# Optimization experiments

Measured on AMD Instinct MI355X. Metric: run time of the kernel, lower is better.

## Reference

```python
import jax, jax.numpy as jnp
import numpy as np

N_STATE, N_OBS, BATCH, T_LEN = 256, 128, 64, 1024
RICCATI_ITERS = 300


def _steady_state_gain(A, H, Q, R, iters=RICCATI_ITERS):
    """Riccati iteration for the steady-state Kalman gain (numpy, fp64)."""
    n = A.shape[0]
    I = np.eye(n)
    P = np.eye(n)
    for _ in range(iters):
        Pp = A @ P @ A.T + Q
        S = H @ Pp @ H.T + R
        K = np.linalg.solve(S, (Pp @ H.T).T).T
        P = (I - K @ H) @ Pp
    return K


def setup_inputs() -> dict:
    rng = np.random.default_rng(0)
    # Stable dynamics: scaled orthogonal matrix (spectral radius 0.95).
    M = rng.standard_normal((N_STATE, N_STATE))
    Qm, _ = np.linalg.qr(M)
    A = 0.95 * Qm
    H = rng.standard_normal((N_OBS, N_STATE)) / np.sqrt(N_STATE)
    Qc = 0.1 * np.eye(N_STATE)
    Rc = 0.1 * np.eye(N_OBS)
    K = _steady_state_gain(A, H, Qc, Rc)

    key = jax.random.key(0)
    y = jax.random.normal(key, (BATCH, T_LEN, N_OBS), dtype=jnp.float32)
    return {
        "y": y,
        "A": jnp.asarray(A, dtype=jnp.float32),
        "H": jnp.asarray(H, dtype=jnp.float32),
        "K": jnp.asarray(K, dtype=jnp.float32),
    }


def reference(y, A, H, K):
    """Steady-state Kalman filter: x_t = (I - K H) A x_{t-1} + K y_t.

    y: [B, T, n_obs] -> out: [B, T, n_state]
    """
    n = A.shape[0]
    I = jnp.eye(n, dtype=A.dtype)
    A_eff = (I - K @ H) @ A  # [n, n]

    x0 = y[:, 0] @ K.T  # [B, n]

    def step(x, yt):
        x = x @ A_eff.T + yt @ K.T  # [B, n]
        return x, x

    ys = jnp.swapaxes(y[:, 1:], 0, 1)  # [T-1, B, n_obs]
    _, xs = jax.lax.scan(step, x0, ys)  # xs: [T-1, B, n]
    out = jnp.concatenate([x0[:, None, :], jnp.swapaxes(xs, 0, 1)], axis=1)
    return out  # [B, T, n_state]
```

## Files before the change

### kernel.cpp

```cpp
#include <hip/hip_runtime.h>

#define NS 256
#define MO 128
#define BB 64
#define TT 1024
#define CCH 64
#define SS 16

typedef short s16x8 __attribute__((ext_vector_type(8)));
typedef float f32x4 __attribute__((ext_vector_type(4)));
typedef unsigned int uint;
typedef unsigned short ushort;

__device__ __forceinline__ ushort f2bf(float x) {
    uint u = __float_as_uint(x);
    uint r = (u + 0x7fffu + ((u >> 16) & 1u)) >> 16;
    return (ushort)r;
}
__device__ __forceinline__ float bf2f(ushort h) { return __uint_as_float(((uint)h) << 16); }

__device__ __forceinline__ f32x4 mfma16(s16x8 a, s16x8 b, f32x4 c) {
    return __builtin_amdgcn_mfma_f32_16x16x32_bf16(a, b, c, 0, 0, 0);
}


__global__ void kh_kernel(const float* __restrict__ K, const float* __restrict__ H,
                          float* __restrict__ KH) {
    int i = blockIdx.x, j = threadIdx.x;
    __shared__ float kl[MO];
    if (j < MO) kl[j] = K[i * MO + j];
    __syncthreads();
    float acc = 0.f;
#pragma unroll 8
    for (int k = 0; k < MO; ++k) acc += kl[k] * H[k * NS + j];
    KH[i * NS + j] = acc;
}

__global__ void aeff_kernel(const float* __restrict__ A, const float* __restrict__ KH,
                            float* __restrict__ AE) {
    int i = blockIdx.x, j = threadIdx.x;
    __shared__ float khr[NS];
    khr[j] = KH[i * NS + j];
    __syncthreads();
    float acc = A[i * NS + j];
#pragma unroll 8
    for (int k = 0; k < NS; ++k) acc -= khr[k] * A[k * NS + j];
    AE[i * NS + j] = acc;
}

__global__ void matsq_kernel(const float* __restrict__ src, float* __restrict__ dst) {
    int i = blockIdx.x, j = threadIdx.x;
    __shared__ float row[NS];
    row[j] = src[i * NS + j];
    __syncthreads();
    float acc = 0.f;
#pragma unroll 8
    for (int k = 0; k < NS; ++k) acc += row[k] * src[k * NS + j];
    dst[i * NS + j] = acc;
}

__global__ void conv_kernel(const float* __restrict__ AE, const float* __restrict__ M,
                            const float* __restrict__ M2,
                            ushort* __restrict__ aeh, ushort* __restrict__ ael,
                            ushort* __restrict__ mh, ushort* __restrict__ ml,
                            ushort* __restrict__ m2h, ushort* __restrict__ m2l) {
    int i = (blockIdx.x & 255) * 256 + threadIdx.x;
    int mat = blockIdx.x >> 8;
    const float* src = (mat == 0) ? AE : ((mat == 1) ? M : M2);
    ushort* dh = (mat == 0) ? aeh : ((mat == 1) ? mh : m2h);
    ushort* dl = (mat == 0) ? ael : ((mat == 1) ? ml : m2l);
    float v = src[i];
    ushort hi = f2bf(v);
    dh[i] = hi;
    dl[i] = f2bf(v - bf2f(hi));
}


__launch_bounds__(512, 2)
__global__ void ugemm_kernel(const float* __restrict__ y, const float* __restrict__ K,
                             float* __restrict__ U) {
    const int tid = threadIdx.x, blk = blockIdx.x;
    const int w = tid >> 6, l = tid & 63, lr = l & 15, lg = l >> 4;

    s16x8 KBh[2][4], KBl[2][4];
#pragma unroll
    for (int t2 = 0; t2 < 2; ++t2) {
        int row = 16 * (2 * w + t2) + lr;
#pragma unroll
        for (int q = 0; q < 4; ++q) {
            int off = row * MO + 32 * q + 8 * lg;
            float4 a = *(const float4*)(K + off);
            float4 b = *(const float4*)(K + off + 4);
            s16x8 vh, vl;
            float f;
            ushort h;
            f = a.x; h = f2bf(f); vh[0] = (short)h; vl[0] = (short)f2bf(f - bf2f(h));
            f = a.y; h = f2bf(f); vh[1] = (short)h; vl[1] = (short)f2bf(f - bf2f(h));
            f = a.z; h = f2bf(f); vh[2] = (short)h; vl[2] = (short)f2bf(f - bf2f(h));
            f = a.w; h = f2bf(f); vh[3] = (short)h; vl[3] = (short)f2bf(f - bf2f(h));
            f = b.x; h = f2bf(f); vh[4] = (short)h; vl[4] = (short)f2bf(f - bf2f(h));
            f = b.y; h = f2bf(f); vh[5] = (short)h; vl[5] = (short)f2bf(f - bf2f(h));
            f = b.z; h = f2bf(f); vh[6] = (short)h; vl[6] = (short)f2bf(f - bf2f(h));
            f = b.w; h = f2bf(f); vh[7] = (short)h; vl[7] = (short)f2bf(f - bf2f(h));
            KBh[t2][q] = vh; KBl[t2][q] = vl;
        }
    }

#pragma unroll 1
    for (int it = 0; it < 16; ++it) {
        int rt = blk * 16 + it;
        s16x8 Ah[4], Al[4];
#pragma unroll
        for (int q = 0; q < 4; ++q) {
            int off = (rt * 16 + lr) * MO + 32 * q + 8 * lg;
            float4 a = *(const float4*)(y + off);
            float4 b = *(const float4*)(y + off + 4);
            s16x8 vh, vl;
            float f;
            ushort h;
            f = a.x; h = f2bf(f); vh[0] = (short)h; vl[0] = (short)f2bf(f - bf2f(h));
            f = a.y; h = f2bf(f); vh[1] = (short)h; vl[1] = (short)f2bf(f - bf2f(h));
            f = a.z; h = f2bf(f); vh[2] = (short)h; vl[2] = (short)f2bf(f - bf2f(h));
            f = a.w; h = f2bf(f); vh[3] = (short)h; vl[3] = (short)f2bf(f - bf2f(h));
            f = b.x; h = f2bf(f); vh[4] = (short)h; vl[4] = (short)f2bf(f - bf2f(h));
            f = b.y; h = f2bf(f); vh[5] = (short)h; vl[5] = (short)f2bf(f - bf2f(h));
            f = b.z; h = f2bf(f); vh[6] = (short)h; vl[6] = (short)f2bf(f - bf2f(h));
            f = b.w; h = f2bf(f); vh[7] = (short)h; vl[7] = (short)f2bf(f - bf2f(h));
            Ah[q] = vh; Al[q] = vl;
        }
        f32x4 acc0 = {0.f, 0.f, 0.f, 0.f};
        f32x4 acc1 = {0.f, 0.f, 0.f, 0.f};
#pragma unroll
        for (int q = 0; q < 4; ++q) {
            acc0 = mfma16(Ah[q], KBh[0][q], acc0);
            acc0 = mfma16(Al[q], KBh[0][q], acc0);
            acc0 = mfma16(Ah[q], KBl[0][q], acc0);
            acc1 = mfma16(Ah[q], KBh[1][q], acc1);
            acc1 = mfma16(Al[q], KBh[1][q], acc1);
            acc1 = mfma16(Ah[q], KBl[1][q], acc1);
        }
#pragma unroll
        for (int i = 0; i < 4; ++i) {
            int orow = rt * 16 + 4 * lg + i;
            U[orow * NS + 32 * w + lr] = acc0[i];
            U[orow * NS + 32 * w + 16 + lr] = acc1[i];
        }
    }
}


template <int MODE>
__launch_bounds__(512, 2)
__global__ void scan16_kernel(const ushort* __restrict__ mh, const ushort* __restrict__ ml,
                              const float* u, const float* __restrict__ cin,
                              float* wout, float* __restrict__ eout) {
    constexpr int S = (MODE == 0 || MODE == 4) ? SS : 8;
    const int tid = threadIdx.x;
    const int blk = blockIdx.x;
    const int w = tid >> 6;
    const int l = tid & 63;
    const int lr = l & 15;
    const int lg = l >> 4;

    __shared__ ushort xh_s[16 * NS];
    __shared__ ushort xl_s[16 * NS];

    auto ubase = [&](int m) -> long {
        if constexpr (MODE == 0 || MODE == 4) {
            int cc = blk >> 2, b = (blk & 3) * 16 + m;
            return ((long)b * TT + cc * SS) * NS;
        } else if constexpr (MODE == 1 || MODE == 3) {
            int rid = blk * 16 + m;
            int b = rid >> 3, g = rid & 7;
            return ((long)b * 64 + g * 8) * NS;
        } else {
            int b = blk * 16 + m;
            return (long)b * 8 * NS;
        }
    };

    s16x8 Bh[2][8], Bl[2][8];
#pragma unroll
    for (int t2 = 0; t2 < 2; ++t2) {
        int row = 16 * (2 * w + t2) + lr;
#pragma unroll
        for (int q = 0; q < 8; ++q) {
            int off = row * NS + 32 * q + 8 * lg;
            Bh[t2][q] = *(const s16x8*)(mh + off);
            Bl[t2][q] = *(const s16x8*)(ml + off);
        }
    }

#pragma unroll
    for (int jj = 0; jj < 8; ++jj) {
        int idx = jj * 512 + tid;
        int m = idx >> 8, col = idx & 255;
        float xv = 0.f;
        if constexpr (MODE == 3) {
            int rid = blk * 16 + m;
            int b = rid >> 3, g = rid & 7;
            xv = cin[(b * 8 + g) * NS + col];
            if (g == 0) wout[(long)b * 64 * NS + col] = 0.f;
        } else if constexpr (MODE == 4) {
            int cc = blk >> 2, b = (blk & 3) * 16 + m;
            xv = cin[(b * 64 + cc) * NS + col];
        } else if constexpr (MODE == 2) {
            int b = blk * 16 + m;
            wout[(long)b * 8 * NS + col] = 0.f;
        }
        ushort hi = f2bf(xv);
        ushort lo = f2bf(xv - bf2f(hi));
        int sidx = (m * NS + col) ^ ((m & 7) << 3);
        xh_s[sidx] = hi;
        xl_s[sidx] = lo;
    }

    const int col0 = 32 * w + lr;
    const int col1 = col0 + 16;

    float up0[4], up1[4];
#pragma unroll
    for (int i = 0; i < 4; ++i) {
        int m = 4 * lg + i;
        long ub = ubase(m);
        up0[i] = u[ub + col0];
        up1[i] = u[ub + col1];
    }
    __syncthreads();

    for (int s = 0; s < S; ++s) {
        f32x4 acc0, acc1;
        acc0[0] = up0[0]; acc0[1] = up0[1]; acc0[2] = up0[2]; acc0[3] = up0[3];
        acc1[0] = up1[0]; acc1[1] = up1[1]; acc1[2] = up1[2]; acc1[3] = up1[3];

#pragma unroll
        for (int q = 0; q < 8; ++q) {
            int ridx = (lr * NS + 32 * q + 8 * lg) ^ ((lr & 7) << 3);
            s16x8 xh = *(const s16x8*)&xh_s[ridx];
            s16x8 xl = *(const s16x8*)&xl_s[ridx];
            acc0 = mfma16(xh, Bh[0][q], acc0);
            acc0 = mfma16(xl, Bh[0][q], acc0);
            acc0 = mfma16(xh, Bl[0][q], acc0);
            acc1 = mfma16(xh, Bh[1][q], acc1);
            acc1 = mfma16(xl, Bh[1][q], acc1);
            acc1 = mfma16(xh, Bl[1][q], acc1);
        }

        if (s + 1 < S) {
#pragma unroll
            for (int i = 0; i < 4; ++i) {
                int m = 4 * lg + i;
                long ub = ubase(m) + (long)(s + 1) * NS;
                up0[i] = u[ub + col0];
                up1[i] = u[ub + col1];
            }
        }

        if constexpr (MODE == 2) {
            if (s < 7) {
#pragma unroll
                for (int i = 0; i < 4; ++i) {
                    int m = 4 * lg + i;
                    int b = blk * 16 + m;
                    long wb = ((long)b * 8 + s + 1) * NS;
                    wout[wb + col0] = acc0[i];
                    wout[wb + col1] = acc1[i];
                }
            }
        } else if constexpr (MODE == 3) {
#pragma unroll
            for (int i = 0; i < 4; ++i) {
                int m = 4 * lg + i;
                int rid = blk * 16 + m;
                int b = rid >> 3, g = rid & 7;
                int kk = 8 * g + s + 1;
                if (kk < 64) {
                    long wb = ((long)b * 64 + kk) * NS;
                    wout[wb + col0] = acc0[i];
                    wout[wb + col1] = acc1[i];
                }
            }
        } else if constexpr (MODE == 4) {
#pragma unroll
            for (int i = 0; i < 4; ++i) {
                int m = 4 * lg + i;
                long wb = ubase(m) + (long)s * NS;
                wout[wb + col0] = acc0[i];
                wout[wb + col1] = acc1[i];
            }
        }
        if constexpr (MODE == 0 || MODE == 1) {
            if (s == S - 1) {
#pragma unroll
                for (int i = 0; i < 4; ++i) {
                    int m = 4 * lg + i;
                    long eb;
                    if constexpr (MODE == 0) {
                        int cc = blk >> 2, b = (blk & 3) * 16 + m;
                        eb = ((long)b * 64 + cc) * NS;
                    } else {
                        eb = (long)(blk * 16 + m) * NS;
                    }
                    eout[eb + col0] = acc0[i];
                    eout[eb + col1] = acc1[i];
                }
            }
        }

        __syncthreads();

#pragma unroll
        for (int i = 0; i < 4; ++i) {
            int m = 4 * lg + i;
            {
                ushort hi = f2bf(acc0[i]);
                ushort lo = f2bf(acc0[i] - bf2f(hi));
                int wi = (m * NS + col0) ^ ((m & 7) << 3);
                xh_s[wi] = hi;
                xl_s[wi] = lo;
            }
            {
                ushort hi = f2bf(acc1[i]);
                ushort lo = f2bf(acc1[i] - bf2f(hi));
                int wi = (m * NS + col1) ^ ((m & 7) << 3);
                xh_s[wi] = hi;
                xl_s[wi] = lo;
            }
        }
        __syncthreads();
    }
}


extern "C" void kernel_launch(void* const* d_in, const int* in_sizes, int n_in,
                              void* d_out, int out_size, void* d_ws, size_t ws_size,
                              hipStream_t stream) {
    const float* y = (const float*)d_in[0];
    const float* A = (const float*)d_in[1];
    const float* H = (const float*)d_in[2];
    const float* K = (const float*)d_in[3];
    float* out = (float*)d_out;

    float* ws = (float*)d_ws;
    const long MAT = (long)NS * NS;
    float* KH = ws + 0 * MAT;
    float* AE = ws + 1 * MAT;
    float* W0 = ws + 2 * MAT;
    float* W1 = ws + 3 * MAT;
    float* W2 = ws + 4 * MAT;
    float* W3 = ws + 5 * MAT;
    float* W4 = ws + 6 * MAT;
    float* W5 = ws + 7 * MAT;
    float* W6 = ws + 8 * MAT;
    ushort* aeh = (ushort*)(ws + 9 * MAT);
    ushort* ael = aeh + MAT;
    ushort* mh = ael + MAT;
    ushort* ml = mh + MAT;
    ushort* m2h = ml + MAT;
    ushort* m2l = m2h + MAT;
    float* e_buf = ws + 12 * MAT;
    float* e2 = ws + 28 * MAT;
    float* c2 = ws + 30 * MAT;
    float* cbuf = ws + 32 * MAT;

    float* U = out;

    kh_kernel<<<NS, NS, 0, stream>>>(K, H, KH);
    aeff_kernel<<<NS, NS, 0, stream>>>(A, KH, AE);
    matsq_kernel<<<NS, NS, 0, stream>>>(AE, W0);
    matsq_kernel<<<NS, NS, 0, stream>>>(W0, W1);
    matsq_kernel<<<NS, NS, 0, stream>>>(W1, W2);
    matsq_kernel<<<NS, NS, 0, stream>>>(W2, W3);
    matsq_kernel<<<NS, NS, 0, stream>>>(W3, W4);
    matsq_kernel<<<NS, NS, 0, stream>>>(W4, W5);
    matsq_kernel<<<NS, NS, 0, stream>>>(W5, W6);
    conv_kernel<<<768, 256, 0, stream>>>(AE, W3, W6, aeh, ael, mh, ml, m2h, m2l);

    ugemm_kernel<<<256, 512, 0, stream>>>(y, K, U);

    scan16_kernel<0><<<256, 512, 0, stream>>>(aeh, ael, U, nullptr, nullptr, e_buf);
    scan16_kernel<1><<<32, 512, 0, stream>>>(mh, ml, e_buf, nullptr, nullptr, e2);
    scan16_kernel<2><<<4, 512, 0, stream>>>(m2h, m2l, e2, nullptr, c2, nullptr);
    scan16_kernel<3><<<32, 512, 0, stream>>>(mh, ml, e_buf, c2, cbuf, nullptr);
    scan16_kernel<4><<<256, 512, 0, stream>>>(aeh, ael, U, cbuf, out, nullptr);
}
```

Measured before the change: 249.5 us.

## Fuse input-projection GEMM into chunked scan kernels, recompute y·Kᵀ on the fly

Removes the separate ugemm kernel that wrote U = y·Kᵀ to the output buffer. The first and last scan passes now stream y into double-buffered shared memory, split it into bf16 hi/lo, and compute the K projection with MFMA before applying the state transition. K is pre-split to bf16 hi/lo once in the conversion kernel. The final pass stages its results in shared memory so it can write them to global memory with coalesced float4 stores. This avoids writing and re-reading the large U tensor and saves a launch, at the cost of doing the projection twice (in both y-consuming passes) and using more shared memory, which may lower occupancy.

```diff
diff --git a/kernel.cpp b/kernel.cpp
--- a/kernel.cpp
+++ b/kernel.cpp
@@ -1,4 +1,5 @@
 #include <hip/hip_runtime.h>
+#include <hip/hip_bf16.h>
 
 #define NS 256
 #define MO 128
@@ -18,6 +19,32 @@
     return (ushort)r;
 }
 __device__ __forceinline__ float bf2f(ushort h) { return __uint_as_float(((uint)h) << 16); }
+
+__device__ __forceinline__ uint pkbf2(float a, float b) {
+    __hip_bfloat162 h = __float22bfloat162_rn(make_float2(a, b));
+    union { __hip_bfloat162 b2; uint u; } cv;
+    cv.b2 = h;
+    return cv.u;
+}
+
+__device__ __forceinline__ void conv8(float4 f0, float4 f1, s16x8& vh, s16x8& vl) {
+    uint h0 = pkbf2(f0.x, f0.y), h1 = pkbf2(f0.z, f0.w);
+    uint h2 = pkbf2(f1.x, f1.y), h3 = pkbf2(f1.z, f1.w);
+    float r0 = f0.x - __uint_as_float(h0 << 16);
+    float r1 = f0.y - __uint_as_float(h0 & 0xffff0000u);
+    float r2 = f0.z - __uint_as_float(h1 << 16);
+    float r3 = f0.w - __uint_as_float(h1 & 0xffff0000u);
+    float r4 = f1.x - __uint_as_float(h2 << 16);
+    float r5 = f1.y - __uint_as_float(h2 & 0xffff0000u);
+    float r6 = f1.z - __uint_as_float(h3 << 16);
+    float r7 = f1.w - __uint_as_float(h3 & 0xffff0000u);
+    uint l0 = pkbf2(r0, r1), l1 = pkbf2(r2, r3);
+    uint l2 = pkbf2(r4, r5), l3 = pkbf2(r6, r7);
+    union { uint u[4]; s16x8 v; } ch, cl;
+    ch.u[0] = h0; ch.u[1] = h1; ch.u[2] = h2; ch.u[3] = h3;
+    cl.u[0] = l0; cl.u[1] = l1; cl.u[2] = l2; cl.u[3] = l3;
+    vh = ch.v; vl = cl.v;
+}
 
 __device__ __forceinline__ f32x4 mfma16(s16x8 a, s16x8 b, f32x4 c) {
     return __builtin_amdgcn_mfma_f32_16x16x32_bf16(a, b, c, 0, 0, 0);
@@ -60,12 +87,22 @@
 }
 
 __global__ void conv_kernel(const float* __restrict__ AE, const float* __restrict__ M,
-                            const float* __restrict__ M2,
+                            const float* __restrict__ M2, const float* __restrict__ K,
                             ushort* __restrict__ aeh, ushort* __restrict__ ael,
                             ushort* __restrict__ mh, ushort* __restrict__ ml,
-                            ushort* __restrict__ m2h, ushort* __restrict__ m2l) {
-    int i = (blockIdx.x & 255) * 256 + threadIdx.x;
-    int mat = blockIdx.x >> 8;
+                            ushort* __restrict__ m2h, ushort* __restrict__ m2l,
+                            ushort* __restrict__ kbh, ushort* __restrict__ kbl) {
+    int blk = blockIdx.x;
+    if (blk >= 768) {
+        int i = (blk - 768) * 256 + threadIdx.x;
+        float v = K[i];
+        ushort hi = f2bf(v);
+        kbh[i] = hi;
+        kbl[i] = f2bf(v - bf2f(hi));
+        return;
+    }
+    int i = (blk & 255) * 256 + threadIdx.x;
+    int mat = blk >> 8;
     const float* src = (mat == 0) ? AE : ((mat == 1) ? M : M2);
     ushort* dh = (mat == 0) ? aeh : ((mat == 1) ? mh : m2h);
     ushort* dl = (mat == 0) ? ael : ((mat == 1) ? ml : m2l);
@@ -76,85 +113,15 @@
 }
 
 
-__launch_bounds__(512, 2)
-__global__ void ugemm_kernel(const float* __restrict__ y, const float* __restrict__ K,
-                             float* __restrict__ U) {
-    const int tid = threadIdx.x, blk = blockIdx.x;
-    const int w = tid >> 6, l = tid & 63, lr = l & 15, lg = l >> 4;
-
-    s16x8 KBh[2][4], KBl[2][4];
-#pragma unroll
-    for (int t2 = 0; t2 < 2; ++t2) {
-        int row = 16 * (2 * w + t2) + lr;
-#pragma unroll
-        for (int q = 0; q < 4; ++q) {
-            int off = row * MO + 32 * q + 8 * lg;
-            float4 a = *(const float4*)(K + off);
-            float4 b = *(const float4*)(K + off + 4);
-            s16x8 vh, vl;
-            float f;
-            ushort h;
-            f = a.x; h = f2bf(f); vh[0] = (short)h; vl[0] = (short)f2bf(f - bf2f(h));
-            f = a.y; h = f2bf(f); vh[1] = (short)h; vl[1] = (short)f2bf(f - bf2f(h));
-            f = a.z; h = f2bf(f); vh[2] = (short)h; vl[2] = (short)f2bf(f - bf2f(h));
-            f = a.w; h = f2bf(f); vh[3] = (short)h; vl[3] = (short)f2bf(f - bf2f(h));
-            f = b.x; h = f2bf(f); vh[4] = (short)h; vl[4] = (short)f2bf(f - bf2f(h));
-            f = b.y; h = f2bf(f); vh[5] = (short)h; vl[5] = (short)f2bf(f - bf2f(h));
-            f = b.z; h = f2bf(f); vh[6] = (short)h; vl[6] = (short)f2bf(f - bf2f(h));
-            f = b.w; h = f2bf(f); vh[7] = (short)h; vl[7] = (short)f2bf(f - bf2f(h));
-            KBh[t2][q] = vh; KBl[t2][q] = vl;
-        }
-    }
-
-#pragma unroll 1
-    for (int it = 0; it < 16; ++it) {
-        int rt = blk * 16 + it;
-        s16x8 Ah[4], Al[4];
-#pragma unroll
-        for (int q = 0; q < 4; ++q) {
-            int off = (rt * 16 + lr) * MO + 32 * q + 8 * lg;
-            float4 a = *(const float4*)(y + off);
-            float4 b = *(const float4*)(y + off + 4);
-            s16x8 vh, vl;
-            float f;
-            ushort h;
-            f = a.x; h = f2bf(f); vh[0] = (short)h; vl[0] = (short)f2bf(f - bf2f(h));
-            f = a.y; h = f2bf(f); vh[1] = (short)h; vl[1] = (short)f2bf(f - bf2f(h));
-            f = a.z; h = f2bf(f); vh[2] = (short)h; vl[2] = (short)f2bf(f - bf2f(h));
-            f = a.w; h = f2bf(f); vh[3] = (short)h; vl[3] = (short)f2bf(f - bf2f(h));
-            f = b.x; h = f2bf(f); vh[4] = (short)h; vl[4] = (short)f2bf(f - bf2f(h));
-            f = b.y; h = f2bf(f); vh[5] = (short)h; vl[5] = (short)f2bf(f - bf2f(h));
-            f = b.z; h = f2bf(f); vh[6] = (short)h; vl[6] = (short)f2bf(f - bf2f(h));
-            f = b.w; h = f2bf(f); vh[7] = (short)h; vl[7] = (short)f2bf(f - bf2f(h));
-            Ah[q] = vh; Al[q] = vl;
-        }
-        f32x4 acc0 = {0.f, 0.f, 0.f, 0.f};
-        f32x4 acc1 = {0.f, 0.f, 0.f, 0.f};
-#pragma unroll
-        for (int q = 0; q < 4; ++q) {
-            acc0 = mfma16(Ah[q], KBh[0][q], acc0);
-            acc0 = mfma16(Al[q], KBh[0][q], acc0);
-            acc0 = mfma16(Ah[q], KBl[0][q], acc0);
-            acc1 = mfma16(Ah[q], KBh[1][q], acc1);
-            acc1 = mfma16(Al[q], KBh[1][q], acc1);
-            acc1 = mfma16(Ah[q], KBl[1][q], acc1);
-        }
-#pragma unroll
-        for (int i = 0; i < 4; ++i) {
-            int orow = rt * 16 + 4 * lg + i;
-            U[orow * NS + 32 * w + lr] = acc0[i];
-            U[orow * NS + 32 * w + 16 + lr] = acc1[i];
-        }
-    }
-}
-
-
 template <int MODE>
 __launch_bounds__(512, 2)
 __global__ void scan16_kernel(const ushort* __restrict__ mh, const ushort* __restrict__ ml,
+                              const ushort* __restrict__ kbh, const ushort* __restrict__ kbl,
+                              const float* __restrict__ y_g,
                               const float* u, const float* __restrict__ cin,
                               float* wout, float* __restrict__ eout) {
-    constexpr int S = (MODE == 0 || MODE == 4) ? SS : 8;
+    constexpr bool YF = (MODE == 0 || MODE == 4);
+    constexpr int S = YF ? SS : 8;
     const int tid = threadIdx.x;
     const int blk = blockIdx.x;
     const int w = tid >> 6;
@@ -164,12 +131,15 @@
 
     __shared__ ushort xh_s[16 * NS];
     __shared__ ushort xl_s[16 * NS];
+    __shared__ float ybuf[2][16 * MO];
+    __shared__ float xe_s[16 * NS];
+
+    const int b0 = (blk & 3) * 16;
+    const int cc = blk >> 2;
+    const int t0 = cc * SS;
 
     auto ubase = [&](int m) -> long {
-        if constexpr (MODE == 0 || MODE == 4) {
-            int cc = blk >> 2, b = (blk & 3) * 16 + m;
-            return ((long)b * TT + cc * SS) * NS;
-        } else if constexpr (MODE == 1 || MODE == 3) {
+        if constexpr (MODE == 1 || MODE == 3) {
             int rid = blk * 16 + m;
             int b = rid >> 3, g = rid & 7;
             return ((long)b * 64 + g * 8) * NS;
@@ -188,6 +158,20 @@
             int off = row * NS + 32 * q + 8 * lg;
             Bh[t2][q] = *(const s16x8*)(mh + off);
             Bl[t2][q] = *(const s16x8*)(ml + off);
+        }
+    }
+
+    s16x8 KBh[2][4], KBl[2][4];
+    if constexpr (YF) {
+#pragma unroll
+        for (int t2 = 0; t2 < 2; ++t2) {
+            int row = 16 * (2 * w + t2) + lr;
+#pragma unroll
+            for (int q = 0; q < 4; ++q) {
+                int off = row * MO + 32 * q + 8 * lg;
+                KBh[t2][q] = *(const s16x8*)(kbh + off);
+                KBl[t2][q] = *(const s16x8*)(kbl + off);
+            }
         }
     }
 
@@ -202,8 +186,7 @@
             xv = cin[(b * 8 + g) * NS + col];
             if (g == 0) wout[(long)b * 64 * NS + col] = 0.f;
         } else if constexpr (MODE == 4) {
-            int cc = blk >> 2, b = (blk & 3) * 16 + m;
-            xv = cin[(b * 64 + cc) * NS + col];
+            xv = cin[((long)(b0 + m) * 64 + cc) * NS + col];
         } else if constexpr (MODE == 2) {
             int b = blk * 16 + m;
             wout[(long)b * 8 * NS + col] = 0.f;
@@ -218,20 +201,55 @@
     const int col0 = 32 * w + lr;
     const int col1 = col0 + 16;
 
+    const int yr = tid >> 5;
+    const int yc = (tid & 31) << 2;
+    const float* ysrc = nullptr;
+    int ywbyte = 0;
+    float4 vnext = make_float4(0.f, 0.f, 0.f, 0.f);
+    if constexpr (YF) {
+        ysrc = y_g + ((size_t)(b0 + yr) * TT + t0) * MO + yc;
+        ywbyte = (yr * 512 + yc * 4) ^ ((yr & 7) << 4);
+        float4 v0 = *(const float4*)(ysrc);
+        *(float4*)((char*)(&ybuf[0][0]) + ywbyte) = v0;
+        vnext = *(const float4*)(ysrc + MO);
+    }
+
     float up0[4], up1[4];
-#pragma unroll
-    for (int i = 0; i < 4; ++i) {
-        int m = 4 * lg + i;
-        long ub = ubase(m);
-        up0[i] = u[ub + col0];
-        up1[i] = u[ub + col1];
+    if constexpr (!YF) {
+#pragma unroll
+        for (int i = 0; i < 4; ++i) {
+            int m = 4 * lg + i;
+            long ub = ubase(m);
+            up0[i] = u[ub + col0];
+            up1[i] = u[ub + col1];
+        }
     }
     __syncthreads();
 
     for (int s = 0; s < S; ++s) {
         f32x4 acc0, acc1;
-        acc0[0] = up0[0]; acc0[1] = up0[1]; acc0[2] = up0[2]; acc0[3] = up0[3];
-        acc1[0] = up1[0]; acc1[1] = up1[1]; acc1[2] = up1[2]; acc1[3] = up1[3];
+        if constexpr (YF) {
+            acc0 = f32x4{0.f, 0.f, 0.f, 0.f};
+            acc1 = f32x4{0.f, 0.f, 0.f, 0.f};
+            const char* yb = (const char*)(&ybuf[s & 1][0]);
+#pragma unroll
+            for (int q = 0; q < 4; ++q) {
+                int lb = lr * 512 + q * 128 + lg * 32;
+                float4 f0 = *(const float4*)(yb + (lb ^ ((lr & 7) << 4)));
+                float4 f1 = *(const float4*)(yb + ((lb + 16) ^ ((lr & 7) << 4)));
+                s16x8 yh, yl;
+                conv8(f0, f1, yh, yl);
+                acc0 = mfma16(yh, KBh[0][q], acc0);
+                acc0 = mfma16(yl, KBh[0][q], acc0);
+                acc0 = mfma16(yh, KBl[0][q], acc0);
+                acc1 = mfma16(yh, KBh[1][q], acc1);
+                acc1 = mfma16(yl, KBh[1][q], acc1);
+                acc1 = mfma16(yh, KBl[1][q], acc1);
+            }
+        } else {
+            acc0[0] = up0[0]; acc0[1] = up0[1]; acc0[2] = up0[2]; acc0[3] = up0[3];
+            acc1[0] = up1[0]; acc1[1] = up1[1]; acc1[2] = up1[2]; acc1[3] = up1[3];
+        }
 
 #pragma unroll
         for (int q = 0; q < 8; ++q) {
@@ -246,13 +264,15 @@
             acc1 = mfma16(xh, Bl[1][q], acc1);
         }
 
-        if (s + 1 < S) {
-#pragma unroll
-            for (int i = 0; i < 4; ++i) {
-                int m = 4 * lg + i;
-                long ub = ubase(m) + (long)(s + 1) * NS;
-                up0[i] = u[ub + col0];
-                up1[i] = u[ub + col1];
+        if constexpr (!YF) {
+            if (s + 1 < S) {
+#pragma unroll
+                for (int i = 0; i < 4; ++i) {
+                    int m = 4 * lg + i;
+                    long ub = ubase(m) + (long)(s + 1) * NS;
+                    up0[i] = u[ub + col0];
+                    up1[i] = u[ub + col1];
+                }
             }
         }
 
@@ -280,14 +300,6 @@
                     wout[wb + col1] = acc1[i];
                 }
             }
-        } else if constexpr (MODE == 4) {
-#pragma unroll
-            for (int i = 0; i < 4; ++i) {
-                int m = 4 * lg + i;
-                long wb = ubase(m) + (long)s * NS;
-                wout[wb + col0] = acc0[i];
-                wout[wb + col1] = acc1[i];
-            }
         }
         if constexpr (MODE == 0 || MODE == 1) {
             if (s == S - 1) {
@@ -296,8 +308,7 @@
                     int m = 4 * lg + i;
                     long eb;
                     if constexpr (MODE == 0) {
-                        int cc = blk >> 2, b = (blk & 3) * 16 + m;
-                        eb = ((long)b * 64 + cc) * NS;
+                        eb = ((long)(b0 + m) * 64 + cc) * NS;
                     } else {
                         eb = (long)(blk * 16 + m) * NS;
                     }
@@ -326,8 +337,30 @@
                 xh_s[wi] = hi;
                 xl_s[wi] = lo;
             }
+            if constexpr (MODE == 4) {
+                xe_s[(m * NS + col0) ^ ((m & 7) << 2)] = acc0[i];
+                xe_s[(m * NS + col1) ^ ((m & 7) << 2)] = acc1[i];
+            }
+        }
+        if constexpr (YF) {
+            if (s + 1 < S) {
+                *(float4*)((char*)(&ybuf[(s + 1) & 1][0]) + ywbyte) = vnext;
+                if (s + 2 < S) vnext = *(const float4*)(ysrc + (size_t)(s + 2) * MO);
+            }
         }
         __syncthreads();
+
+        if constexpr (MODE == 4) {
+#pragma unroll
+            for (int j = 0; j < 2; ++j) {
+                int idx = j * 512 + tid;
+                int r = idx >> 6;
+                int wb = idx << 2;
+                float4 vv = *(const float4*)&xe_s[wb ^ ((r & 7) << 2)];
+                long ob = ((long)(b0 + r) * TT + (t0 + s)) * NS + (wb & 255);
+                *(float4*)(wout + ob) = vv;
+            }
+        }
     }
 }
 
@@ -358,12 +391,12 @@
     ushort* ml = mh + MAT;
     ushort* m2h = ml + MAT;
     ushort* m2l = m2h + MAT;
-    float* e_buf = ws + 12 * MAT;
-    float* e2 = ws + 28 * MAT;
-    float* c2 = ws + 30 * MAT;
-    float* cbuf = ws + 32 * MAT;
-
-    float* U = out;
+    ushort* kbh = (ushort*)(ws + 12 * MAT);
+    ushort* kbl = kbh + (long)NS * MO;
+    float* e_buf = ws + 13 * MAT;
+    float* e2 = ws + 29 * MAT;
+    float* c2 = ws + 31 * MAT;
+    float* cbuf = ws + 33 * MAT;
 
     kh_kernel<<<NS, NS, 0, stream>>>(K, H, KH);
     aeff_kernel<<<NS, NS, 0, stream>>>(A, KH, AE);
@@ -374,13 +407,11 @@
     matsq_kernel<<<NS, NS, 0, stream>>>(W3, W4);
     matsq_kernel<<<NS, NS, 0, stream>>>(W4, W5);
     matsq_kernel<<<NS, NS, 0, stream>>>(W5, W6);
-    conv_kernel<<<768, 256, 0, stream>>>(AE, W3, W6, aeh, ael, mh, ml, m2h, m2l);
-
-    ugemm_kernel<<<256, 512, 0, stream>>>(y, K, U);
-
-    scan16_kernel<0><<<256, 512, 0, stream>>>(aeh, ael, U, nullptr, nullptr, e_buf);
-    scan16_kernel<1><<<32, 512, 0, stream>>>(mh, ml, e_buf, nullptr, nullptr, e2);
-    scan16_kernel<2><<<4, 512, 0, stream>>>(m2h, m2l, e2, nullptr, c2, nullptr);
-    scan16_kernel<3><<<32, 512, 0, stream>>>(mh, ml, e_buf, c2, cbuf, nullptr);
-    scan16_kernel<4><<<256, 512, 0, stream>>>(aeh, ael, U, cbuf, out, nullptr);
-}
+    conv_kernel<<<896, 256, 0, stream>>>(AE, W3, W6, K, aeh, ael, mh, ml, m2h, m2l, kbh, kbl);
+
+    scan16_kernel<0><<<256, 512, 0, stream>>>(aeh, ael, kbh, kbl, y, nullptr, nullptr, nullptr, e_buf);
+    scan16_kernel<1><<<32, 512, 0, stream>>>(mh, ml, nullptr, nullptr, nullptr, e_buf, nullptr, nullptr, e2);
+    scan16_kernel<2><<<4, 512, 0, stream>>>(m2h, m2l, nullptr, nullptr, nullptr, e2, nullptr, c2, nullptr);
+    scan16_kernel<3><<<32, 512, 0, stream>>>(mh, ml, nullptr, nullptr, nullptr, e_buf, c2, cbuf, nullptr);
+    scan16_kernel<4><<<256, 512, 0, stream>>>(aeh, ael, kbh, kbl, y, nullptr, cbuf, out, nullptr);
+}
```

After: 272.4 us. +9.2%, slower.
